# Kernel optimization log

Measured on AMD Instinct MI355X. Metric: run time of the kernel, lower is better.

Reference implementation:

```python
import jax, jax.numpy as jnp
import numpy as np

N = 50000
E = 400000
IN_DIM = 128
HID = 128
OUT = 128
HEADS = 8
NEG_SLOPE = 0.2  # PyG GATConv default
BN_EPS = 1e-5


def _gat_conv(x, W, a_src, a_dst, b, src, dst, concat):
    """PyG GATConv (eval): self-loops added by caller. x:[N,F], W:[F,H*C], a_*:[H,C]."""
    H, C = a_src.shape
    xW = (x @ W).reshape(N, H, C)                       # [N,H,C]
    es = jnp.sum(xW * a_src[None], axis=-1)             # [N,H]
    ed = jnp.sum(xW * a_dst[None], axis=-1)             # [N,H]
    e = jax.nn.leaky_relu(es[src] + ed[dst], NEG_SLOPE) # [E,H]
    m = jax.ops.segment_max(e, dst, num_segments=N)     # softmax over incoming edges per dst
    ex = jnp.exp(e - m[dst])
    denom = jax.ops.segment_sum(ex, dst, num_segments=N)
    alpha = ex / denom[dst]                             # [E,H]
    out = jax.ops.segment_sum(xW[src] * alpha[:, :, None], dst, num_segments=N)  # [N,H,C]
    out = out.reshape(N, H * C) if concat else out.mean(axis=1)
    return out + b


def _bn_eval(h, g, be, rm, rv):
    return (h - rm) * jax.lax.rsqrt(rv + BN_EPS) * g + be


def setup_inputs() -> dict:
    key = jax.random.key(0)
    ks = jax.random.split(key, 20)
    C1 = HID // HEADS
    f32 = jnp.float32
    inp = {
        "x": jax.random.normal(ks[0], (N, IN_DIM), dtype=f32),
        "edge_index": jax.random.randint(ks[1], (2, E), 0, N, dtype=jnp.int64),
        # GAT layer 1 (in->hid, 8 heads, concat)
        "W1": jax.random.normal(ks[2], (IN_DIM, HEADS * C1), dtype=f32) * 0.05,
        "a_src1": jax.random.normal(ks[3], (HEADS, C1), dtype=f32) * 0.05,
        "a_dst1": jax.random.normal(ks[4], (HEADS, C1), dtype=f32) * 0.05,
        "b1": jnp.zeros((HEADS * C1,), dtype=f32),
        # GAT layer 2 (hid->hid, 8 heads, concat)
        "W2": jax.random.normal(ks[5], (HID, HEADS * C1), dtype=f32) * 0.05,
        "a_src2": jax.random.normal(ks[6], (HEADS, C1), dtype=f32) * 0.05,
        "a_dst2": jax.random.normal(ks[7], (HEADS, C1), dtype=f32) * 0.05,
        "b2": jnp.zeros((HEADS * C1,), dtype=f32),
        # GAT layer 3 (hid->out, 1 head, no concat)
        "W3": jax.random.normal(ks[8], (HID, OUT), dtype=f32) * 0.05,
        "a_src3": jax.random.normal(ks[9], (1, OUT), dtype=f32) * 0.05,
        "a_dst3": jax.random.normal(ks[10], (1, OUT), dtype=f32) * 0.05,
        "b3": jnp.zeros((OUT,), dtype=f32),
        # residual linears
        "R1w": jax.random.normal(ks[11], (IN_DIM, HID), dtype=f32) * 0.05,
        "R1b": jnp.zeros((HID,), dtype=f32),
        "R2w": jax.random.normal(ks[12], (HID, HID), dtype=f32) * 0.05,
        "R2b": jnp.zeros((HID,), dtype=f32),
        "R3w": jax.random.normal(ks[13], (HID, OUT), dtype=f32) * 0.05,
        "R3b": jnp.zeros((OUT,), dtype=f32),
        # batch norms (eval mode: running stats)
        "g1": jnp.ones((HID,), dtype=f32), "be1": jnp.zeros((HID,), dtype=f32),
        "rm1": jnp.zeros((HID,), dtype=f32), "rv1": jnp.ones((HID,), dtype=f32),
        "g2": jnp.ones((HID,), dtype=f32), "be2": jnp.zeros((HID,), dtype=f32),
        "rm2": jnp.zeros((HID,), dtype=f32), "rv2": jnp.ones((HID,), dtype=f32),
    }
    return inp


def reference(x, edge_index, W1, a_src1, a_dst1, b1, W2, a_src2, a_dst2, b2,
              W3, a_src3, a_dst3, b3, R1w, R1b, R2w, R2b, R3w, R3b,
              g1, be1, rm1, rv1, g2, be2, rm2, rv2):
    # PyG GATConv adds self-loops by default
    loops = jnp.arange(N, dtype=edge_index.dtype)
    src = jnp.concatenate([edge_index[0], loops])
    dst = jnp.concatenate([edge_index[1], loops])

    h = _gat_conv(x, W1, a_src1, a_dst1, b1, src, dst, concat=True) + (x @ R1w + R1b)
    h1 = jax.nn.relu(_bn_eval(h, g1, be1, rm1, rv1))  # dropout identity in eval

    h = _gat_conv(h1, W2, a_src2, a_dst2, b2, src, dst, concat=True) + (h1 @ R2w + R2b)
    h2 = jax.nn.relu(_bn_eval(h, g2, be2, rm2, rv2))

    out = _gat_conv(h2, W3, a_src3, a_dst3, b3, src, dst, concat=False) + (h2 @ R3w + R3b)
    return out
```

## Files before the change

kernel.cpp:

```cpp
#include <hip/hip_runtime.h>
#include <hip/hip_bf16.h>
#include <type_traits>

typedef __hip_bfloat16 bf16;
typedef __hip_bfloat162 bf162;
typedef short v8s __attribute__((ext_vector_type(8)));
typedef float v4f __attribute__((ext_vector_type(4)));

#define CAP 64

__device__ __forceinline__ float lrelu(float x) { return x > 0.f ? x : 0.2f * x; }
__device__ __forceinline__ float b2f(bf16 v) { return __bfloat162float(v); }

__global__ void k_preW(const float* __restrict__ s0, const float* __restrict__ s1,
                       const float* __restrict__ s2, const float* __restrict__ s3,
                       const float* __restrict__ s4, const float* __restrict__ s5,
                       const float* __restrict__ as1, const float* __restrict__ ad1,
                       const float* __restrict__ as2, const float* __restrict__ ad2,
                       const float* __restrict__ as3, const float* __restrict__ ad3,
                       const float* b1, const float* R1b, const float* g1, const float* be1,
                       const float* rm1, const float* rv1,
                       const float* b2, const float* R2b, const float* g2, const float* be2,
                       const float* rm2, const float* rv2,
                       const float* b3, const float* R3b,
                       bf16* __restrict__ wt, float* __restrict__ prm,
                       int* __restrict__ cnt, int N) {
    int b = blockIdx.x;
    int t = threadIdx.x;
    if (b >= 7) {
        int n4 = N * 4;
        int base = ((b - 7) * 256 + t) * 4;
        int4 z = {0, 0, 0, 0};
#pragma unroll
        for (int k = 0; k < 4; ++k)
            if (base + k < n4) ((int4*)cnt)[base + k] = z;
        return;
    }
    if (b == 6) {
        int c = t;
        if (c < 128) {
            float s1v = g1[c] * rsqrtf(rv1[c] + 1e-5f);
            prm[c]       = b1[c] + R1b[c];
            prm[128 + c] = s1v;
            prm[256 + c] = be1[c] - rm1[c] * s1v;
            float s2v = g2[c] * rsqrtf(rv2[c] + 1e-5f);
            prm[384 + c] = b2[c] + R2b[c];
            prm[512 + c] = s2v;
            prm[640 + c] = be2[c] - rm2[c] * s2v;
            prm[768 + c] = b3[c] + R3b[c];
        }
        return;
    }
    const float* src;
    switch (b) {
        case 0: src = s0; break; case 1: src = s1; break; case 2: src = s2; break;
        case 3: src = s3; break; case 4: src = s4; break; default: src = s5; break;
    }
    bf16* dst = wt + (size_t)b * 18432;
    for (int i = t; i < 16384; i += 256) {
        int k = i >> 7, n = i & 127;
        dst[n * 128 + k] = __float2bfloat16(src[i]);
    }
    if ((b & 1) == 0) {
        int layer = b >> 1;
        if (layer < 2) {
            const float* asr = (layer == 0) ? as1 : as2;
            const float* ads = (layer == 0) ? ad1 : ad2;
            for (int i = t; i < 2048; i += 256) {
                int row = i >> 7, k = i & 127, h = row & 7;
                const float* av = (row < 8) ? asr : ads;
                float s = 0.f;
#pragma unroll
                for (int c = 0; c < 16; ++c) s += src[k * 128 + h * 16 + c] * av[h * 16 + c];
                dst[(128 + row) * 128 + k] = __float2bfloat16(s);
            }
        } else {
            for (int i = t; i < 2048; i += 256) {
                int row = i >> 7, k = i & 127;
                float s = 0.f;
                if (row == 0 || row == 8) {
                    const float* av = (row == 0) ? as3 : ad3;
                    for (int c = 0; c < 128; ++c) s += src[k * 128 + c] * av[c];
                }
                dst[(128 + row) * 128 + k] = __float2bfloat16(s);
            }
        }
    } else {
        for (int i = t; i < 2048; i += 256)
            dst[16384 + i] = __float2bfloat16(0.f);
    }
}

template <typename T>
__device__ __forceinline__ void gemm_body(const T* __restrict__ A,
                                          const bf16* __restrict__ BT0, const bf16* __restrict__ BT1,
                                          bf16* __restrict__ O0, bf16* __restrict__ O1,
                                          float* __restrict__ es, float* __restrict__ ed,
                                          int mode, int nrows, int job, int ntiles,
                                          bf16* Bsh) {
    const int y = (job >= ntiles) ? 1 : 0;
    const int tile = y ? job - ntiles : job;
    const bf16* BT = y ? BT1 : BT0;
    bf16* O = y ? O1 : O0;
    const int t = threadIdx.x;
    const int rowbase = tile * 128;
    const int wave = t >> 6, lane = t & 63, quad = lane >> 4, l16 = lane & 15;

    int gra[2];
    gra[0] = rowbase + wave * 32 + l16;      if (gra[0] >= nrows) gra[0] = nrows - 1;
    gra[1] = rowbase + wave * 32 + 16 + l16; if (gra[1] >= nrows) gra[1] = nrows - 1;
    v8s afr[2][4];
    if constexpr (std::is_same<T, float>::value) {
#pragma unroll
        for (int rt = 0; rt < 2; ++rt) {
            const float* arow = A + (size_t)gra[rt] * 128 + quad * 8;
#pragma unroll
            for (int kit = 0; kit < 4; ++kit) {
                float4 u = *(const float4*)(arow + kit * 32);
                float4 w = *(const float4*)(arow + kit * 32 + 4);
                union { bf16 h[8]; v8s v; } tmp;
                tmp.h[0] = __float2bfloat16(u.x); tmp.h[1] = __float2bfloat16(u.y);
                tmp.h[2] = __float2bfloat16(u.z); tmp.h[3] = __float2bfloat16(u.w);
                tmp.h[4] = __float2bfloat16(w.x); tmp.h[5] = __float2bfloat16(w.y);
                tmp.h[6] = __float2bfloat16(w.z); tmp.h[7] = __float2bfloat16(w.w);
                afr[rt][kit] = tmp.v;
            }
        }
    } else {
#pragma unroll
        for (int rt = 0; rt < 2; ++rt) {
            const bf16* arow = A + (size_t)gra[rt] * 128 + quad * 8;
#pragma unroll
            for (int kit = 0; kit < 4; ++kit)
                afr[rt][kit] = *(const v8s*)(arow + kit * 32);
        }
    }

    for (int s = t; s < 288; s += 256) {
        int r = s >> 1, hf = s & 1;
        const float4* bsrc = (const float4*)(BT + r * 128 + hf * 64);
#pragma unroll
        for (int j = 0; j < 8; ++j) {
            int c = hf * 8 + j, cp = c ^ (r & 7);
            *(float4*)(&Bsh[r * 128 + cp * 8]) = bsrc[j];
        }
    }
    __syncthreads();

    v4f acc[2][9];
#pragma unroll
    for (int i = 0; i < 2; ++i)
#pragma unroll
        for (int j = 0; j < 9; ++j) acc[i][j] = (v4f){0.f, 0.f, 0.f, 0.f};
#pragma unroll
    for (int kit = 0; kit < 4; ++kit) {
        v8s bfr[9];
#pragma unroll
        for (int ct = 0; ct < 9; ++ct) {
            int nn = ct * 16 + l16;
            int cp = (kit * 4 + quad) ^ (nn & 7);
            bfr[ct] = *(const v8s*)(&Bsh[nn * 128 + cp * 8]);
        }
#pragma unroll
        for (int rt = 0; rt < 2; ++rt)
#pragma unroll
            for (int ct = 0; ct < 9; ++ct)
                acc[rt][ct] = __builtin_amdgcn_mfma_f32_16x16x32_bf16(afr[rt][kit], bfr[ct], acc[rt][ct], 0, 0, 0);
    }
#pragma unroll
    for (int rt = 0; rt < 2; ++rt)
#pragma unroll
        for (int ct = 0; ct < 8; ++ct)
#pragma unroll
            for (int r = 0; r < 4; ++r) {
                int gr = rowbase + wave * 32 + rt * 16 + quad * 4 + r;
                if (gr < nrows) O[(size_t)gr * 128 + ct * 16 + l16] = __float2bfloat16(acc[rt][ct][r]);
            }
    if (mode != 0 && y == 0) {
#pragma unroll
        for (int rt = 0; rt < 2; ++rt)
#pragma unroll
            for (int r = 0; r < 4; ++r) {
                int gr = rowbase + wave * 32 + rt * 16 + quad * 4 + r;
                if (gr < nrows) {
                    float v = acc[rt][8][r];
                    if (mode == 1) {
                        if (l16 < 8) es[(size_t)gr * 8 + l16] = v;
                        else         ed[(size_t)gr * 8 + (l16 - 8)] = v;
                    } else {
                        if (l16 == 0) es[gr] = v;
                        else if (l16 == 8) ed[gr] = v;
                    }
                }
            }
    }
}

__global__ void k_fillgemm(const float* __restrict__ A,
                           const bf16* __restrict__ BT0, const bf16* __restrict__ BT1,
                           bf16* __restrict__ O0, bf16* __restrict__ O1,
                           float* __restrict__ es, float* __restrict__ ed,
                           int nrows, int ntiles,
                           const int* __restrict__ ei, int* __restrict__ cnt,
                           int* __restrict__ csr, int E) {
    __shared__ bf16 Bsh[144 * 128];
    const int njobs = 2 * ntiles;
    if (blockIdx.x < njobs) {
        gemm_body<float>(A, BT0, BT1, O0, O1, es, ed, 1, nrows, blockIdx.x, ntiles, Bsh);
        return;
    }
    int base = (blockIdx.x - njobs) * 1024 + threadIdx.x * 4;
    if (base >= E) return;
    if (((E & 3) == 0) && base + 3 < E) {
        int4 s4 = *(const int4*)(ei + base);
        int4 d4 = *(const int4*)(ei + E + base);
        int p0 = atomicAdd(&cnt[(size_t)d4.x * 16], 1);
        int p1 = atomicAdd(&cnt[(size_t)d4.y * 16], 1);
        int p2 = atomicAdd(&cnt[(size_t)d4.z * 16], 1);
        int p3 = atomicAdd(&cnt[(size_t)d4.w * 16], 1);
        if (p0 < CAP) csr[d4.x * CAP + p0] = s4.x;
        if (p1 < CAP) csr[d4.y * CAP + p1] = s4.y;
        if (p2 < CAP) csr[d4.z * CAP + p2] = s4.z;
        if (p3 < CAP) csr[d4.w * CAP + p3] = s4.w;
    } else {
        for (int i = base; i < E && i < base + 4; ++i) {
            int d = ei[E + i];
            int pos = atomicAdd(&cnt[(size_t)d * 16], 1);
            if (pos < CAP) csr[d * CAP + pos] = ei[i];
        }
    }
}

__global__ void k_gemm(const bf16* __restrict__ A,
                       const bf16* __restrict__ BT0, const bf16* __restrict__ BT1,
                       bf16* __restrict__ O0, bf16* __restrict__ O1,
                       float* __restrict__ es, float* __restrict__ ed,
                       int mode, int nrows, int ntiles) {
    __shared__ bf16 Bsh[144 * 128];
    gemm_body<bf16>(A, BT0, BT1, O0, O1, es, ed, mode, nrows, blockIdx.x, ntiles, Bsh);
}

__global__ void k_agg8(const bf16* __restrict__ xW, const float* __restrict__ es8,
                       const float* __restrict__ ed8,
                       const int* __restrict__ cnt, const int* __restrict__ csr,
                       const bf16* __restrict__ rres, const float* __restrict__ prm,
                       bf16* __restrict__ hout, int n) {
    int wave = threadIdx.x >> 6, lane = threadIdx.x & 63;
    int node = blockIdx.x * 4 + wave;
    if (node >= n) return;
    const int g = lane >> 4, l16 = lane & 15;
    const int c0 = l16 * 8;
    const int hc = l16 >> 1;
    const int he = lane & 7;
    float edw = ed8[(size_t)node * 8 + he];
    float wselfh = __expf(lrelu(es8[(size_t)node * 8 + he] + edw));
    float acc[8]; float den = 0.f;
    v8s rv;
#pragma unroll
    for (int i = 0; i < 8; ++i) acc[i] = 0.f;
    {
        float ws = __shfl(wselfh, hc);
        if (g == 0) {
            rv = *(const v8s*)(rres + (size_t)node * 128 + c0);
            v8s xv = *(const v8s*)(xW + (size_t)node * 128 + c0);
            const bf16* xb = (const bf16*)&xv;
            den = ws;
#pragma unroll
            for (int i = 0; i < 8; ++i) acc[i] = ws * b2f(xb[i]);
        }
    }
    int deg = cnt[(size_t)node * 16]; if (deg > CAP) deg = CAP;
    const int* bucket = csr + (size_t)node * CAP;
    int idx = (lane < deg) ? bucket[lane] : node;
    for (int sub = 0; sub * 8 < deg; ++sub) {
        int j0 = sub * 8 + g, j1 = sub * 8 + 4 + g;
        int sv0 = __shfl(idx, j0);
        int sv1 = __shfl(idx, j1);
        v8s xv0 = *(const v8s*)(xW + (size_t)sv0 * 128 + c0);
        v8s xv1 = *(const v8s*)(xW + (size_t)sv1 * 128 + c0);
        int e = sub * 8 + (lane >> 3);
        int sidx = __shfl(idx, e);
        float esv = es8[(size_t)sidx * 8 + he];
        float w = (e < deg) ? __expf(lrelu(esv + edw)) : 0.f;
        float w0 = __shfl(w, g * 8 + hc);
        float w1 = __shfl(w, (4 + g) * 8 + hc);
        const bf16* xb0 = (const bf16*)&xv0;
        const bf16* xb1 = (const bf16*)&xv1;
        den += w0 + w1;
#pragma unroll
        for (int i = 0; i < 8; ++i) acc[i] += w0 * b2f(xb0[i]) + w1 * b2f(xb1[i]);
    }
    den += __shfl_xor(den, 16); den += __shfl_xor(den, 32);
#pragma unroll
    for (int i = 0; i < 8; ++i) {
        acc[i] += __shfl_xor(acc[i], 16);
        acc[i] += __shfl_xor(acc[i], 32);
    }
    if (g == 0) {
        float inv = 1.f / den;
        const bf16* rb = (const bf16*)&rv;
        bf16 outv[8];
#pragma unroll
        for (int i = 0; i < 8; ++i) {
            int c = c0 + i;
            float v = acc[i] * inv + prm[c] + b2f(rb[i]);
            v = fmaxf(v * prm[128 + c] + prm[256 + c], 0.f);
            outv[i] = __float2bfloat16(v);
        }
        *(v8s*)(hout + (size_t)node * 128 + c0) = *(v8s*)outv;
    }
}

__global__ void k_agg1(const bf16* __restrict__ xW, const float* __restrict__ es,
                       const float* __restrict__ ed,
                       const int* __restrict__ cnt, const int* __restrict__ csr,
                       const bf16* __restrict__ rres, const float* __restrict__ bias,
                       float* __restrict__ out, int n) {
    int wave = threadIdx.x >> 6, lane = threadIdx.x & 63;
    int node = blockIdx.x * 4 + wave;
    if (node >= n) return;
    const int g = lane >> 4, l16 = lane & 15;
    const int c0 = l16 * 8;
    float edv = ed[node];
    float wself = __expf(lrelu(es[node] + edv));
    float acc[8]; float den = 0.f;
    v8s rv;
#pragma unroll
    for (int i = 0; i < 8; ++i) acc[i] = 0.f;
    if (g == 0) {
        rv = *(const v8s*)(rres + (size_t)node * 128 + c0);
        v8s xv = *(const v8s*)(xW + (size_t)node * 128 + c0);
        const bf16* xb = (const bf16*)&xv;
        den = wself;
#pragma unroll
        for (int i = 0; i < 8; ++i) acc[i] = wself * b2f(xb[i]);
    }
    int deg = cnt[(size_t)node * 16]; if (deg > CAP) deg = CAP;
    const int* bucket = csr + (size_t)node * CAP;
    int idx = (lane < deg) ? bucket[lane] : node;
    float w = (lane < deg) ? __expf(lrelu(es[idx] + edv)) : 0.f;
    for (int j = 0; j < deg; j += 4) {
        int jl = j + g;
        int sv = __shfl(idx, jl);
        float wj = __shfl(w, jl);
        if (jl >= deg) wj = 0.f;
        v8s xv = *(const v8s*)(xW + (size_t)sv * 128 + c0);
        const bf16* xb = (const bf16*)&xv;
        den += wj;
#pragma unroll
        for (int i = 0; i < 8; ++i) acc[i] += wj * b2f(xb[i]);
    }
    den += __shfl_xor(den, 16); den += __shfl_xor(den, 32);
#pragma unroll
    for (int i = 0; i < 8; ++i) {
        acc[i] += __shfl_xor(acc[i], 16);
        acc[i] += __shfl_xor(acc[i], 32);
    }
    if (g == 0) {
        float inv = 1.f / den;
        const bf16* rb = (const bf16*)&rv;
        float ov[8];
#pragma unroll
        for (int i = 0; i < 8; ++i)
            ov[i] = acc[i] * inv + bias[c0 + i] + b2f(rb[i]);
        float4 o0, o1;
        o0.x = ov[0]; o0.y = ov[1]; o0.z = ov[2]; o0.w = ov[3];
        o1.x = ov[4]; o1.y = ov[5]; o1.z = ov[6]; o1.w = ov[7];
        *(float4*)(out + (size_t)node * 128 + c0) = o0;
        *(float4*)(out + (size_t)node * 128 + c0 + 4) = o1;
    }
}

extern "C" void kernel_launch(void* const* d_in, const int* in_sizes, int n_in,
                              void* d_out, int out_size, void* d_ws, size_t ws_size,
                              hipStream_t stream) {
    const float* x   = (const float*)d_in[0];
    const int*   ei  = (const int*)d_in[1];
    const float* W1  = (const float*)d_in[2];
    const float* as1 = (const float*)d_in[3];
    const float* ad1 = (const float*)d_in[4];
    const float* b1  = (const float*)d_in[5];
    const float* W2  = (const float*)d_in[6];
    const float* as2 = (const float*)d_in[7];
    const float* ad2 = (const float*)d_in[8];
    const float* b2  = (const float*)d_in[9];
    const float* W3  = (const float*)d_in[10];
    const float* as3 = (const float*)d_in[11];
    const float* ad3 = (const float*)d_in[12];
    const float* b3  = (const float*)d_in[13];
    const float* R1w = (const float*)d_in[14];
    const float* R1b = (const float*)d_in[15];
    const float* R2w = (const float*)d_in[16];
    const float* R2b = (const float*)d_in[17];
    const float* R3w = (const float*)d_in[18];
    const float* R3b = (const float*)d_in[19];
    const float* g1  = (const float*)d_in[20];
    const float* be1 = (const float*)d_in[21];
    const float* rm1 = (const float*)d_in[22];
    const float* rv1 = (const float*)d_in[23];
    const float* g2  = (const float*)d_in[24];
    const float* be2 = (const float*)d_in[25];
    const float* rm2 = (const float*)d_in[26];
    const float* rv2 = (const float*)d_in[27];

    const int N = in_sizes[0] / 128;
    const int E = in_sizes[1] / 2;

    char* p = (char*)d_ws;
    size_t off = 0;
    auto alloc = [&](size_t b) { void* r = p + off; off = (off + b + 255) & ~(size_t)255; return r; };
    int*   cnt  = (int*)alloc((size_t)N * 16 * 4);
    int*   csr  = (int*)alloc((size_t)N * CAP * 4);
    bf16*  WT   = (bf16*)alloc((size_t)6 * 18432 * 2);
    float* prm  = (float*)alloc(896 * 4);
    float* es   = (float*)alloc((size_t)N * 8 * 4);
    float* ed   = (float*)alloc((size_t)N * 8 * 4);
    bf16*  xW   = (bf16*)alloc((size_t)N * 128 * 2);
    bf16*  rres = (bf16*)alloc((size_t)N * 128 * 2);
    bf16*  hA   = (bf16*)alloc((size_t)N * 128 * 2);
    bf16*  hB   = (bf16*)alloc((size_t)N * 128 * 2);
    (void)ws_size; (void)n_in; (void)out_size;

    const int gx = (N + 127) / 128;
    const int nw = (N + 3) / 4;
    const int fb = (E + 1023) / 1024;
    const int zb = (N * 4 + 1023) / 1024;

    k_preW<<<7 + zb, 256, 0, stream>>>(W1, R1w, W2, R2w, W3, R3w,
                                       as1, ad1, as2, ad2, as3, ad3,
                                       b1, R1b, g1, be1, rm1, rv1,
                                       b2, R2b, g2, be2, rm2, rv2, b3, R3b,
                                       WT, prm, cnt, N);
    k_fillgemm<<<2 * gx + fb, 256, 0, stream>>>(x, WT, WT + 18432, xW, rres, es, ed,
                                                N, gx, ei, cnt, csr, E);
    k_agg8<<<nw, 256, 0, stream>>>(xW, es, ed, cnt, csr, rres, prm, hA, N);
    k_gemm<<<2 * gx, 256, 0, stream>>>(hA, WT + 2 * 18432, WT + 3 * 18432, xW, rres, es, ed, 1, N, gx);
    k_agg8<<<nw, 256, 0, stream>>>(xW, es, ed, cnt, csr, rres, prm + 384, hB, N);
    k_gemm<<<2 * gx, 256, 0, stream>>>(hB, WT + 4 * 18432, WT + 5 * 18432, xW, rres, es, ed, 2, N, gx);
    k_agg1<<<nw, 256, 0, stream>>>(xW, es, ed, cnt, csr, rres, prm + 768, (float*)d_out, N);
}
```

Before: 313.2 us.

## Inline small adjacency in count slots, interleave es/ed, vectorize GEMM epilogue stores

```diff
diff --git a/kernel.cpp b/kernel.cpp
--- a/kernel.cpp
+++ b/kernel.cpp
@@ -5,6 +5,7 @@
 typedef __hip_bfloat16 bf16;
 typedef __hip_bfloat162 bf162;
 typedef short v8s __attribute__((ext_vector_type(8)));
+typedef short v4s __attribute__((ext_vector_type(4)));
 typedef float v4f __attribute__((ext_vector_type(4)));
 
 #define CAP 64
@@ -95,7 +96,8 @@
 __device__ __forceinline__ void gemm_body(const T* __restrict__ A,
                                           const bf16* __restrict__ BT0, const bf16* __restrict__ BT1,
                                           bf16* __restrict__ O0, bf16* __restrict__ O1,
-                                          float* __restrict__ es, float* __restrict__ ed,
+                                          float* __restrict__ esed, float* __restrict__ es,
+                                          float* __restrict__ ed,
                                           int mode, int nrows, int job, int ntiles,
                                           bf16* Bsh) {
     const int y = (job >= ntiles) ? 1 : 0;
@@ -106,14 +108,14 @@
     const int rowbase = tile * 128;
     const int wave = t >> 6, lane = t & 63, quad = lane >> 4, l16 = lane & 15;
 
-    int gra[2];
-    gra[0] = rowbase + wave * 32 + l16;      if (gra[0] >= nrows) gra[0] = nrows - 1;
-    gra[1] = rowbase + wave * 32 + 16 + l16; if (gra[1] >= nrows) gra[1] = nrows - 1;
+    int gr[2], grc[2];
+    gr[0] = rowbase + wave * 32 + l16;      grc[0] = gr[0] < nrows ? gr[0] : nrows - 1;
+    gr[1] = gr[0] + 16;                     grc[1] = gr[1] < nrows ? gr[1] : nrows - 1;
     v8s afr[2][4];
     if constexpr (std::is_same<T, float>::value) {
 #pragma unroll
         for (int rt = 0; rt < 2; ++rt) {
-            const float* arow = A + (size_t)gra[rt] * 128 + quad * 8;
+            const float* arow = A + (size_t)grc[rt] * 128 + quad * 8;
 #pragma unroll
             for (int kit = 0; kit < 4; ++kit) {
                 float4 u = *(const float4*)(arow + kit * 32);
@@ -129,7 +131,7 @@
     } else {
 #pragma unroll
         for (int rt = 0; rt < 2; ++rt) {
-            const bf16* arow = A + (size_t)gra[rt] * 128 + quad * 8;
+            const bf16* arow = A + (size_t)grc[rt] * 128 + quad * 8;
 #pragma unroll
             for (int kit = 0; kit < 4; ++kit)
                 afr[rt][kit] = *(const v8s*)(arow + kit * 32);
@@ -165,83 +167,78 @@
         for (int rt = 0; rt < 2; ++rt)
 #pragma unroll
             for (int ct = 0; ct < 9; ++ct)
-                acc[rt][ct] = __builtin_amdgcn_mfma_f32_16x16x32_bf16(afr[rt][kit], bfr[ct], acc[rt][ct], 0, 0, 0);
-    }
-#pragma unroll
-    for (int rt = 0; rt < 2; ++rt)
-#pragma unroll
-        for (int ct = 0; ct < 8; ++ct)
-#pragma unroll
-            for (int r = 0; r < 4; ++r) {
-                int gr = rowbase + wave * 32 + rt * 16 + quad * 4 + r;
-                if (gr < nrows) O[(size_t)gr * 128 + ct * 16 + l16] = __float2bfloat16(acc[rt][ct][r]);
-            }
-    if (mode != 0 && y == 0) {
-#pragma unroll
-        for (int rt = 0; rt < 2; ++rt)
-#pragma unroll
-            for (int r = 0; r < 4; ++r) {
-                int gr = rowbase + wave * 32 + rt * 16 + quad * 4 + r;
-                if (gr < nrows) {
-                    float v = acc[rt][8][r];
-                    if (mode == 1) {
-                        if (l16 < 8) es[(size_t)gr * 8 + l16] = v;
-                        else         ed[(size_t)gr * 8 + (l16 - 8)] = v;
-                    } else {
-                        if (l16 == 0) es[gr] = v;
-                        else if (l16 == 8) ed[gr] = v;
-                    }
-                }
-            }
+                acc[rt][ct] = __builtin_amdgcn_mfma_f32_16x16x32_bf16(bfr[ct], afr[rt][kit], acc[rt][ct], 0, 0, 0);
+    }
+#pragma unroll
+    for (int rt = 0; rt < 2; ++rt) {
+        if (gr[rt] < nrows) {
+            bf16* orow = O + (size_t)gr[rt] * 128 + quad * 4;
+#pragma unroll
+            for (int ct = 0; ct < 8; ++ct) {
+                union { bf16 h[4]; v4s v; } pk;
+#pragma unroll
+                for (int r = 0; r < 4; ++r) pk.h[r] = __float2bfloat16(acc[rt][ct][r]);
+                *(v4s*)(orow + ct * 16) = pk.v;
+            }
+            if (mode == 1 && y == 0) {
+                *(v4f*)(esed + (size_t)gr[rt] * 16 + quad * 4) = acc[rt][8];
+            } else if (mode == 2 && y == 0) {
+                if (quad == 0) es[gr[rt]] = acc[rt][8][0];
+                else if (quad == 2) ed[gr[rt]] = acc[rt][8][0];
+            }
+        }
     }
 }
 
 __global__ void k_fillgemm(const float* __restrict__ A,
                            const bf16* __restrict__ BT0, const bf16* __restrict__ BT1,
                            bf16* __restrict__ O0, bf16* __restrict__ O1,
-                           float* __restrict__ es, float* __restrict__ ed,
-                           int nrows, int ntiles,
+                           float* __restrict__ esed, float* __restrict__ es, float* __restrict__ ed,
+                           int nrows, int ntiles, int fb,
                            const int* __restrict__ ei, int* __restrict__ cnt,
                            int* __restrict__ csr, int E) {
     __shared__ bf16 Bsh[144 * 128];
-    const int njobs = 2 * ntiles;
-    if (blockIdx.x < njobs) {
-        gemm_body<float>(A, BT0, BT1, O0, O1, es, ed, 1, nrows, blockIdx.x, ntiles, Bsh);
+    if (blockIdx.x < fb) {
+        int base = blockIdx.x * 1024 + threadIdx.x * 4;
+        if (base >= E) return;
+        if (((E & 3) == 0) && base + 3 < E) {
+            int4 s4 = *(const int4*)(ei + base);
+            int4 d4 = *(const int4*)(ei + E + base);
+            int p0 = atomicAdd(&cnt[(size_t)d4.x * 16], 1);
+            int p1 = atomicAdd(&cnt[(size_t)d4.y * 16], 1);
+            int p2 = atomicAdd(&cnt[(size_t)d4.z * 16], 1);
+            int p3 = atomicAdd(&cnt[(size_t)d4.w * 16], 1);
+            if (p0 < 15) cnt[(size_t)d4.x * 16 + 1 + p0] = s4.x;
+            else if (p0 < CAP) csr[d4.x * CAP + p0] = s4.x;
+            if (p1 < 15) cnt[(size_t)d4.y * 16 + 1 + p1] = s4.y;
+            else if (p1 < CAP) csr[d4.y * CAP + p1] = s4.y;
+            if (p2 < 15) cnt[(size_t)d4.z * 16 + 1 + p2] = s4.z;
+            else if (p2 < CAP) csr[d4.z * CAP + p2] = s4.z;
+            if (p3 < 15) cnt[(size_t)d4.w * 16 + 1 + p3] = s4.w;
+            else if (p3 < CAP) csr[d4.w * CAP + p3] = s4.w;
+        } else {
+            for (int i = base; i < E && i < base + 4; ++i) {
+                int d = ei[E + i];
+                int pos = atomicAdd(&cnt[(size_t)d * 16], 1);
+                if (pos < 15) cnt[(size_t)d * 16 + 1 + pos] = ei[i];
+                else if (pos < CAP) csr[d * CAP + pos] = ei[i];
+            }
+        }
         return;
     }
-    int base = (blockIdx.x - njobs) * 1024 + threadIdx.x * 4;
-    if (base >= E) return;
-    if (((E & 3) == 0) && base + 3 < E) {
-        int4 s4 = *(const int4*)(ei + base);
-        int4 d4 = *(const int4*)(ei + E + base);
-        int p0 = atomicAdd(&cnt[(size_t)d4.x * 16], 1);
-        int p1 = atomicAdd(&cnt[(size_t)d4.y * 16], 1);
-        int p2 = atomicAdd(&cnt[(size_t)d4.z * 16], 1);
-        int p3 = atomicAdd(&cnt[(size_t)d4.w * 16], 1);
-        if (p0 < CAP) csr[d4.x * CAP + p0] = s4.x;
-        if (p1 < CAP) csr[d4.y * CAP + p1] = s4.y;
-        if (p2 < CAP) csr[d4.z * CAP + p2] = s4.z;
-        if (p3 < CAP) csr[d4.w * CAP + p3] = s4.w;
-    } else {
-        for (int i = base; i < E && i < base + 4; ++i) {
-            int d = ei[E + i];
-            int pos = atomicAdd(&cnt[(size_t)d * 16], 1);
-            if (pos < CAP) csr[d * CAP + pos] = ei[i];
-        }
-    }
+    gemm_body<float>(A, BT0, BT1, O0, O1, esed, es, ed, 1, nrows, blockIdx.x - fb, ntiles, Bsh);
 }
 
 __global__ void k_gemm(const bf16* __restrict__ A,
                        const bf16* __restrict__ BT0, const bf16* __restrict__ BT1,
                        bf16* __restrict__ O0, bf16* __restrict__ O1,
-                       float* __restrict__ es, float* __restrict__ ed,
+                       float* __restrict__ esed, float* __restrict__ es, float* __restrict__ ed,
                        int mode, int nrows, int ntiles) {
     __shared__ bf16 Bsh[144 * 128];
-    gemm_body<bf16>(A, BT0, BT1, O0, O1, es, ed, mode, nrows, blockIdx.x, ntiles, Bsh);
-}
-
-__global__ void k_agg8(const bf16* __restrict__ xW, const float* __restrict__ es8,
-                       const float* __restrict__ ed8,
+    gemm_body<bf16>(A, BT0, BT1, O0, O1, esed, es, ed, mode, nrows, blockIdx.x, ntiles, Bsh);
+}
+
+__global__ void k_agg8(const bf16* __restrict__ xW, const float* __restrict__ esed,
                        const int* __restrict__ cnt, const int* __restrict__ csr,
                        const bf16* __restrict__ rres, const float* __restrict__ prm,
                        bf16* __restrict__ hout, int n) {
@@ -252,8 +249,8 @@
     const int c0 = l16 * 8;
     const int hc = l16 >> 1;
     const int he = lane & 7;
-    float edw = ed8[(size_t)node * 8 + he];
-    float wselfh = __expf(lrelu(es8[(size_t)node * 8 + he] + edw));
+    float edw = esed[(size_t)node * 16 + 8 + he];
+    float wselfh = __expf(lrelu(esed[(size_t)node * 16 + he] + edw));
     float acc[8]; float den = 0.f;
     v8s rv;
 #pragma unroll
@@ -270,8 +267,9 @@
         }
     }
     int deg = cnt[(size_t)node * 16]; if (deg > CAP) deg = CAP;
-    const int* bucket = csr + (size_t)node * CAP;
-    int idx = (lane < deg) ? bucket[lane] : node;
+    int idx = node;
+    if (lane < deg)
+        idx = (lane < 15) ? cnt[(size_t)node * 16 + 1 + lane] : csr[(size_t)node * CAP + lane];
     for (int sub = 0; sub * 8 < deg; ++sub) {
         int j0 = sub * 8 + g, j1 = sub * 8 + 4 + g;
         int sv0 = __shfl(idx, j0);
@@ -280,7 +278,7 @@
         v8s xv1 = *(const v8s*)(xW + (size_t)sv1 * 128 + c0);
         int e = sub * 8 + (lane >> 3);
         int sidx = __shfl(idx, e);
-        float esv = es8[(size_t)sidx * 8 + he];
+        float esv = esed[(size_t)sidx * 16 + he];
         float w = (e < deg) ? __expf(lrelu(esv + edw)) : 0.f;
         float w0 = __shfl(w, g * 8 + hc);
         float w1 = __shfl(w, (4 + g) * 8 + hc);
@@ -336,8 +334,9 @@
         for (int i = 0; i < 8; ++i) acc[i] = wself * b2f(xb[i]);
     }
     int deg = cnt[(size_t)node * 16]; if (deg > CAP) deg = CAP;
-    const int* bucket = csr + (size_t)node * CAP;
-    int idx = (lane < deg) ? bucket[lane] : node;
+    int idx = node;
+    if (lane < deg)
+        idx = (lane < 15) ? cnt[(size_t)node * 16 + 1 + lane] : csr[(size_t)node * CAP + lane];
     float w = (lane < deg) ? __expf(lrelu(es[idx] + edv)) : 0.f;
     for (int j = 0; j < deg; j += 4) {
         int jl = j + g;
@@ -413,8 +412,9 @@
     int*   csr  = (int*)alloc((size_t)N * CAP * 4);
     bf16*  WT   = (bf16*)alloc((size_t)6 * 18432 * 2);
     float* prm  = (float*)alloc(896 * 4);
-    float* es   = (float*)alloc((size_t)N * 8 * 4);
-    float* ed   = (float*)alloc((size_t)N * 8 * 4);
+    float* esed = (float*)alloc((size_t)N * 16 * 4);
+    float* es   = (float*)alloc((size_t)N * 4);
+    float* ed   = (float*)alloc((size_t)N * 4);
     bf16*  xW   = (bf16*)alloc((size_t)N * 128 * 2);
     bf16*  rres = (bf16*)alloc((size_t)N * 128 * 2);
     bf16*  hA   = (bf16*)alloc((size_t)N * 128 * 2);
@@ -431,11 +431,11 @@
                                        b1, R1b, g1, be1, rm1, rv1,
                                        b2, R2b, g2, be2, rm2, rv2, b3, R3b,
                                        WT, prm, cnt, N);
-    k_fillgemm<<<2 * gx + fb, 256, 0, stream>>>(x, WT, WT + 18432, xW, rres, es, ed,
-                                                N, gx, ei, cnt, csr, E);
-    k_agg8<<<nw, 256, 0, stream>>>(xW, es, ed, cnt, csr, rres, prm, hA, N);
-    k_gemm<<<2 * gx, 256, 0, stream>>>(hA, WT + 2 * 18432, WT + 3 * 18432, xW, rres, es, ed, 1, N, gx);
-    k_agg8<<<nw, 256, 0, stream>>>(xW, es, ed, cnt, csr, rres, prm + 384, hB, N);
-    k_gemm<<<2 * gx, 256, 0, stream>>>(hB, WT + 4 * 18432, WT + 5 * 18432, xW, rres, es, ed, 2, N, gx);
+    k_fillgemm<<<fb + 2 * gx, 256, 0, stream>>>(x, WT, WT + 18432, xW, rres, esed, es, ed,
+                                                N, gx, fb, ei, cnt, csr, E);
+    k_agg8<<<nw, 256, 0, stream>>>(xW, esed, cnt, csr, rres, prm, hA, N);
+    k_gemm<<<2 * gx, 256, 0, stream>>>(hA, WT + 2 * 18432, WT + 3 * 18432, xW, rres, esed, es, ed, 1, N, gx);
+    k_agg8<<<nw, 256, 0, stream>>>(xW, esed, cnt, csr, rres, prm + 384, hB, N);
+    k_gemm<<<2 * gx, 256, 0, stream>>>(hB, WT + 4 * 18432, WT + 5 * 18432, xW, rres, esed, es, ed, 2, N, gx);
     k_agg1<<<nw, 256, 0, stream>>>(xW, es, ed, cnt, csr, rres, prm + 768, (float*)d_out, N);
 }
```

Result: slower. 335.8 us (+7.2%).
